# Performance work log

Hardware: AMD Instinct MI355X
Metric: run time of the kernel (lower is better)

Reference implementation:

```python
import jax, jax.numpy as jnp
import numpy as np

jax.config.update("jax_enable_x64", True)  # original torch code runs in float64; minors underflow fp32

D = 96   # Nsites
N = 48   # Nparticles


def setup_inputs() -> dict:
    key = jax.random.key(0)
    # Orthonormal single-particle orbitals (columns), as the module assumes (P^T P = I)
    A = jax.random.normal(key, (D, D), dtype=jnp.float64)
    Q, _ = jnp.linalg.qr(A)
    P = Q[:, :N]  # [D, N]
    # A valid ordered particle configuration: strictly increasing, occ_positions[k] <= D-N+k
    occ_positions = jnp.arange(N, dtype=jnp.int32) * (D // N)  # stride-2 filling
    return {"P": P, "occ_positions": occ_positions}


def _cond_probs(P, occ_positions):
    """Conditional probabilities probs[k, x] of placing the k-th (ordered) particle at
    site x given particles 0..k-1 at occ_positions[0..k-1].

    Math identical to SlaterDetSampler_ordered.get_cond_prob (naive_update=True):
      G = I - P P^T
      probs[k,x] = -det(M_x[0:x+1,0:x+1]) / det(M[0:xmin,0:xmin])
    where M = G - diag(occupancy of particles < k) and M_x additionally sets n_x = 1.
    Since Ksites is always the contiguous range 0..x, all determinants are LEADING
    principal minors; and because only the (x,x) diagonal entry changes by -1 (last index
    of the block), det(M_x block) = d_{x+1} - d_x with d_j the leading j-minor of M.
    """
    Dd, Nn = P.shape
    dt = P.dtype
    eye = jnp.eye(Dd, dtype=dt)
    G = eye - P @ P.T                                             # [D, D]

    onehots = jax.nn.one_hot(occ_positions, Dd, dtype=dt)         # [N, D]
    n_before = jnp.cumsum(onehots, axis=0) - onehots              # occupancy of particles < k
    A = G[None] - n_before[:, :, None] * eye                      # [N, D, D]: G - diag(n_<k)

    # All leading principal minors via batched det of masked matrices:
    # M_j = A on the [0:j,0:j] block, identity elsewhere  =>  det(M_j) = leading j-minor
    ii = jnp.arange(Dd)
    jj = jnp.arange(1, Dd + 1)
    blk = (ii[None, :, None] < jj[:, None, None]) & (ii[None, None, :] < jj[:, None, None])  # [D,D,D]
    Ms = jnp.where(blk[None], A[:, None], eye)                    # [N, D, D, D]
    d = jnp.linalg.det(Ms.reshape(Nn * Dd, Dd, Dd)).reshape(Nn, Dd)
    d_full = jnp.concatenate([jnp.ones((Nn, 1), dt), d], axis=1)  # d_full[k, j] = j-th leading minor

    k = jnp.arange(Nn)
    xmin = jnp.where(k == 0, 0, occ_positions[jnp.maximum(k - 1, 0)] + 1)  # [N]
    xmax = Dd - Nn + k + 1                                                  # [N]
    denom = jnp.take_along_axis(d_full, xmin[:, None], axis=1)              # [N, 1]
    num = d_full[:, 1:] - d_full[:, :-1]                                    # det(GG_num) per candidate x

    x = jnp.arange(Dd)
    support = (x[None, :] >= xmin[:, None]) & (x[None, :] < xmax[:, None])
    probs = jnp.where(support, -num / denom, jnp.zeros((), dt))
    # torch.where(abs(probs) > 1e-15, probs, 0.)
    probs = jnp.where(jnp.abs(probs) > 1e-15, probs, jnp.zeros((), dt))
    return probs


def reference(P, occ_positions):
    probs = _cond_probs(P, occ_positions)                          # [N, D]
    # prob of the full ordered sample = prod_k probs[k, occ_positions[k]]  (as in sample())
    p_k = jnp.take_along_axis(probs, occ_positions[:, None], axis=1)[:, 0]
    prob_sample = jnp.prod(p_k)
    return probs, prob_sample
```

## Files before the change

kernel.cpp:

```cpp
#include <hip/hip_runtime.h>
#include <math.h>

#define Dd 96
#define Nn 48
#define LD 97
#define PTS 98
#define WS_G_BYTES (Dd * Dd * 8)

__device__ __forceinline__ double frcp(double x) {
    double r = __builtin_amdgcn_rcp(x);
    r = fma(fma(-x, r, 1.0), r, r);
    r = fma(fma(-x, r, 1.0), r, r);
    return r;
}

__device__ __forceinline__ double rdlane(double v, int srcLane) {
    union { double d; int i[2]; } u; u.d = v;
    int lo = __builtin_amdgcn_readlane(u.i[0], srcLane);
    int hi = __builtin_amdgcn_readlane(u.i[1], srcLane);
    union { int i[2]; double d; } w; w.i[0] = lo; w.i[1] = hi;
    return w.d;
}

__global__ __launch_bounds__(256) void build_g(const float* __restrict__ P,
                                               double* __restrict__ Mg) {
    __shared__ float Ps[Dd * 48];
    const int t0 = threadIdx.x;
    for (int e = t0; e < Dd * 48; e += 256) Ps[e] = P[e];
    __syncthreads();
    const int e = blockIdx.x * 256 + t0;
    const int r = e / Dd, c = e - Dd * (e / Dd);
    const float* pr = Ps + r * 48;
    const float* pc = Ps + c * 48;
    double acc = 0.0;
#pragma unroll
    for (int t = 0; t < 48; ++t)
        acc -= (double)pr[t] * (double)pc[t];
    Mg[e] = acc;
}

__global__ __launch_bounds__(1024, 1) void slater_elim(const double* __restrict__ Mg,
                                                       const int* __restrict__ occ,
                                                       float* __restrict__ out,
                                                       unsigned* __restrict__ cnt) {
    __shared__ double Sbuf[4][6][Dd];
    __shared__ double ev16[16][6];
    __shared__ int    evmask16[16], sdead16[16];
    __shared__ double evm[6];
    __shared__ int    evmmask;
    __shared__ double gs_runprod;
    __shared__ int    gs_dead;
    __shared__ int    step_pub;
    __shared__ int    done4[4];
    __shared__ unsigned char flag[Dd];

    const int tid  = threadIdx.x;
    const int k    = blockIdx.x;
    const int n    = Dd - Nn + k + 1;
    const int lane = tid & 63;
    const int wave = tid >> 6;
    const int xmin = (k == 0) ? 0 : occ[k - 1] + 1;
    const int s_end = (n - 1) / 6;
    const int jend  = 6 * s_end;

    if (tid == 0) { step_pub = -1; gs_runprod = 1.0; gs_dead = 0; evmmask = 0; }
    if (tid < 4)  done4[tid] = 0;
    if (tid < 16) { evmask16[tid] = 0; sdead16[tid] = 0; }
    if (tid < Dd) flag[tid] = 0;
    __syncthreads();
    if (tid < k) flag[occ[tid]] = 1;
    __syncthreads();

    double myprob = 0.0;
    double rr[6][2];

#pragma unroll
    for (int u = 0; u < 6; ++u) {
        if (lane < 48) {
            const int row = 6 * wave + u;
            double2 g = *(const double2*)(Mg + row * Dd + 2 * lane);
            double d0 = (row == 2 * lane     && !flag[row]) ? 1.0 : 0.0;
            double d1 = (row == 2 * lane + 1 && !flag[row]) ? 1.0 : 0.0;
            rr[u][0] = g.x + d0;
            rr[u][1] = g.y + d1;
        } else { rr[u][0] = 0.0; rr[u][1] = 0.0; }
    }

    auto prefactor = [&](int p, int slot) {
        const int jb = 6 * p, jbH = 3 * p;
        double grun = gs_runprod; int gdead = gs_dead;
        int msk = 0;
#pragma unroll
        for (int cc = 0; cc < 6; ++cc) {
            const int src = jbH + (cc >> 1);
            double piv = rdlane(rr[cc][cc & 1], src);
            if (!gdead) {
                double ap = fabs(piv);
                int jj = jb + cc;
                if (jj >= xmin) {
                    if (lane == 0) ev16[p][cc] = grun * (1.0 - piv);
                    msk |= (1 << cc);
                    double nr = grun * piv;
                    if (!(ap > 1e-7) || !(ap < 8.0) || !(fabs(nr) > 1e-8)) gdead = 1;
                    else grun = nr;
                } else {
                    if (!(ap > 1e-12) || !(ap < 8.0)) gdead = 1;
                }
            }
            double rp = frcp(piv);
            rr[cc][0] *= rp; rr[cc][1] *= rp;
            if (cc < 5) {
                double f = rdlane(rr[cc + 1][cc & 1], src);
                rr[cc + 1][0] -= f * rr[cc][0];
                rr[cc + 1][1] -= f * rr[cc][1];
            }
#pragma unroll
            for (int i = 0; i < 6; ++i) {
                if (i == cc || i == cc + 1) continue;
                double f = rdlane(rr[i][cc & 1], src);
                rr[i][0] -= f * rr[cc][0];
                rr[i][1] -= f * rr[cc][1];
            }
        }
        if (lane == 0) {
            evmask16[p] = msk; sdead16[p] = gdead;
            gs_runprod = grun; gs_dead = gdead;
        }
        if (lane < 48) {
            const bool live = (2 * lane >= jb + 6);
#pragma unroll
            for (int r = 0; r < 6; ++r) {
                double2 sv;
                sv.x = live ? rr[r][0] : 0.0;
                sv.y = live ? rr[r][1] : 0.0;
                *(double2*)&Sbuf[slot][r][2 * lane] = sv;
            }
        }
        __threadfence_block();
        if (lane == 0)
            __hip_atomic_store(&step_pub, p, __ATOMIC_RELEASE, __HIP_MEMORY_SCOPE_WORKGROUP);
    };

    if (wave == 0) prefactor(0, 0);

    bool broke = false;
    const int smax = (wave < s_end) ? wave : s_end;
    for (int s = 0; s < smax; ++s) {
        while (__hip_atomic_load(&step_pub, __ATOMIC_ACQUIRE,
                                 __HIP_MEMORY_SCOPE_WORKGROUP) < s)
            __builtin_amdgcn_s_sleep(1);
        if (sdead16[s]) { broke = true; break; }
        const int slot = s & 3;
        double S0[6], S1[6];
        if (lane < 48) {
#pragma unroll
            for (int r = 0; r < 6; ++r) {
                double2 sv = *(const double2*)&Sbuf[slot][r][2 * lane];
                S0[r] = sv.x; S1[r] = sv.y;
            }
            const int al = 3 * s;
#pragma unroll
            for (int u = 0; u < 6; ++u) {
#pragma unroll
                for (int r = 0; r < 6; ++r) {
                    double a = rdlane(rr[u][r & 1], al + (r >> 1));
                    rr[u][0] -= a * S0[r];
                    rr[u][1] -= a * S1[r];
                }
            }
        }
        if (lane == 0)
            __hip_atomic_fetch_add(&done4[slot], 1, __ATOMIC_RELEASE,
                                   __HIP_MEMORY_SCOPE_WORKGROUP);
        if (wave == s + 1 && s + 1 < s_end) {
            const int p = s + 1;
            if (p >= 4) {
                const int q = p & 3, m = p >> 2;
                const int T = m * (15 - q) - 2 * m * (m - 1);
                while (__hip_atomic_load(&done4[q], __ATOMIC_ACQUIRE,
                                         __HIP_MEMORY_SCOPE_WORKGROUP) < T)
                    __builtin_amdgcn_s_sleep(1);
            }
            prefactor(p, p & 3);
        }
    }

    if (!broke && wave == s_end) {
        const int rsz = n - jend;
        double grun = gs_runprod; int gdead = gs_dead;
        int msk = 0;
#pragma unroll
        for (int cc = 0; cc < 6; ++cc) {
            const int src = 3 * s_end + (cc >> 1);
            double piv = rdlane(rr[cc][cc & 1], src);
            double evv = 0.0;
            if (cc < rsz - 1) {
                if (!gdead) {
                    double ap = fabs(piv);
                    int jj = jend + cc;
                    if (jj >= xmin) {
                        evv = grun * (1.0 - piv); msk |= (1 << cc);
                        double nr = grun * piv;
                        if (!(ap > 1e-7) || !(ap < 8.0) || !(fabs(nr) > 1e-8)) gdead = 1;
                        else grun = nr;
                    } else {
                        if (!(ap > 1e-12) || !(ap < 8.0)) gdead = 1;
                    }
                }
            } else if (cc == rsz - 1) {
                if (!gdead) { evv = grun * (1.0 - piv); msk |= (1 << cc); }
            }
            if (lane == 0) evm[cc] = evv;
            double rp = frcp(piv);
            rr[cc][0] *= rp; rr[cc][1] *= rp;
            if (cc < 5) {
                double f = rdlane(rr[cc + 1][cc & 1], src);
                rr[cc + 1][0] -= f * rr[cc][0];
                rr[cc + 1][1] -= f * rr[cc][1];
            }
#pragma unroll
            for (int i = 0; i < 6; ++i) {
                if (i == cc || i == cc + 1) continue;
                double f = rdlane(rr[i][cc & 1], src);
                rr[i][0] -= f * rr[cc][0];
                rr[i][1] -= f * rr[cc][1];
            }
        }
        if (lane == 0) evmmask = msk;
    }
    __syncthreads();

    if (tid < jend) {
        int sp = tid / 6, q = tid - 6 * sp;
        if ((evmask16[sp] >> q) & 1) myprob = ev16[sp][q];
    } else if (tid < n) {
        int q = tid - jend;
        if ((evmmask >> q) & 1) myprob = evm[q];
    }

    if (tid < Dd) {
        double p = myprob;
        if (!isfinite(p)) p = 0.0;
        if (!(fabs(p) > 1e-15)) p = 0.0;
        p = fmin(fmax(p, 0.0), 1.0);
        out[k * Dd + tid] = (float)p;
    }

    __threadfence();
    __syncthreads();
    if (wave == 0) {
        int old = 0;
        if (lane == 0)
            old = (int)__hip_atomic_fetch_add(cnt, 1u, __ATOMIC_ACQ_REL,
                                              __HIP_MEMORY_SCOPE_AGENT);
        old = __shfl(old, 0, 64);
        if (((unsigned)old + 1u) % (unsigned)Nn == 0u) {
            __threadfence();
            double v = 1.0;
            if (lane < Nn) {
                float f = __hip_atomic_load(out + lane * Dd + occ[lane],
                                            __ATOMIC_RELAXED, __HIP_MEMORY_SCOPE_AGENT);
                v = (double)f;
            }
#pragma unroll
            for (int off = 32; off >= 1; off >>= 1)
                v *= __shfl_down(v, off, 64);
            if (lane == 0) {
                if (!isfinite(v)) v = 0.0;
                out[Nn * Dd] = (float)v;
            }
        }
    }
}

__global__ __launch_bounds__(1024, 1) void slater_mono(const float* __restrict__ P,
                                                       const int* __restrict__ occ,
                                                       float* __restrict__ out,
                                                       unsigned* __restrict__ cnt) {
    __shared__ double As[Dd * LD];
    __shared__ double Sbuf[4][6][Dd];
    __shared__ double ev16[16][6];
    __shared__ int    evmask16[16], sdead16[16];
    __shared__ double evm[6];
    __shared__ int    evmmask;
    __shared__ double gs_runprod;
    __shared__ int    gs_dead;
    __shared__ int    step_pub;
    __shared__ int    done4[4];
    __shared__ unsigned char flag[Dd];
    float* PT = (float*)As;

    const int tid  = threadIdx.x;
    const int k    = blockIdx.x;
    const int n    = Dd - Nn + k + 1;
    const int lane = tid & 63;
    const int wave = tid >> 6;
    const int xmin = (k == 0) ? 0 : occ[k - 1] + 1;
    const int s_end = (n - 1) / 6;
    const int jend  = 6 * s_end;

    if (tid == 0) { step_pub = -1; gs_runprod = 1.0; gs_dead = 0; evmmask = 0; }
    if (tid < 4)  done4[tid] = 0;
    if (tid < 16) { evmask16[tid] = 0; sdead16[tid] = 0; }
    if (tid < Dd) flag[tid] = 0;
    __syncthreads();
    if (tid < k) flag[occ[tid]] = 1;
    for (int e = tid; e < Dd * Nn; e += 1024) {
        int c = e / Nn, t = e - (e / Nn) * Nn;
        PT[t * PTS + c] = P[e];
    }
    __syncthreads();

    double Areg[8]; int trs[2], tcs[2];
#pragma unroll
    for (int it = 0; it < 2; ++it) {
        int tau = tid + 1024 * it;
        double s00 = 0.0, s01 = 0.0, s10 = 0.0, s11 = 0.0;
        int tr = 0, tc = 0;
        if (tau < 1176) {
            tr = (int)((97.0 - sqrt(9409.0 - 8.0 * (double)tau)) * 0.5);
            while ((tr * (97 - tr)) / 2 > tau) --tr;
            while (((tr + 1) * (96 - tr)) / 2 <= tau) ++tr;
            tc = tr + (tau - (tr * (97 - tr)) / 2);
            int r0 = 2 * tr, c0 = 2 * tc;
            if (r0 < n && c0 < n) {
                for (int t = 0; t < Nn; ++t) {
                    const float* row = PT + t * PTS;
                    float2 pr = *(const float2*)(row + r0);
                    float2 pc = *(const float2*)(row + c0);
                    s00 -= (double)pr.x * (double)pc.x; s01 -= (double)pr.x * (double)pc.y;
                    s10 -= (double)pr.y * (double)pc.x; s11 -= (double)pr.y * (double)pc.y;
                }
            }
        }
        trs[it] = tr; tcs[it] = tc;
        Areg[it * 4 + 0] = s00; Areg[it * 4 + 1] = s01;
        Areg[it * 4 + 2] = s10; Areg[it * 4 + 3] = s11;
    }
    __syncthreads();
#pragma unroll
    for (int it = 0; it < 2; ++it) {
        int tau = tid + 1024 * it;
        if (tau < 1176) {
            int tr = trs[it], tc = tcs[it];
            int r0 = 2 * tr, c0 = 2 * tc;
            if (r0 < n && c0 < n) {
                bool r1 = (r0 + 1 < n), c1 = (c0 + 1 < n);
                double d0 = flag[r0] ? 0.0 : 1.0;
                double d1 = flag[r0 + 1] ? 0.0 : 1.0;
                As[r0 * LD + c0] = Areg[it * 4 + 0] + ((r0 == c0) ? d0 : 0.0);
                if (c1)       As[r0 * LD + c0 + 1]       = Areg[it * 4 + 1];
                if (r1)       As[(r0 + 1) * LD + c0]     = Areg[it * 4 + 2];
                if (r1 && c1) As[(r0 + 1) * LD + c0 + 1] = Areg[it * 4 + 3] + ((r0 == c0) ? d1 : 0.0);
                if (tr != tc) {
                    As[c0 * LD + r0] = Areg[it * 4 + 0];
                    if (c1)       As[(c0 + 1) * LD + r0]     = Areg[it * 4 + 1];
                    if (r1)       As[c0 * LD + r0 + 1]       = Areg[it * 4 + 2];
                    if (r1 && c1) As[(c0 + 1) * LD + r0 + 1] = Areg[it * 4 + 3];
                }
            }
        }
    }
    __syncthreads();

    double myprob = 0.0;
    double rr[6][2];
#pragma unroll
    for (int u = 0; u < 6; ++u) {
        if (lane < 48) {
            rr[u][0] = As[(6 * wave + u) * LD + 2 * lane];
            rr[u][1] = As[(6 * wave + u) * LD + 2 * lane + 1];
        } else { rr[u][0] = 0.0; rr[u][1] = 0.0; }
    }

    auto prefactor = [&](int p, int slot) {
        const int jb = 6 * p, jbH = 3 * p;
        double grun = gs_runprod; int gdead = gs_dead;
        int msk = 0;
#pragma unroll
        for (int cc = 0; cc < 6; ++cc) {
            const int src = jbH + (cc >> 1);
            double piv = rdlane(rr[cc][cc & 1], src);
            if (!gdead) {
                double ap = fabs(piv);
                int jj = jb + cc;
                if (jj >= xmin) {
                    if (lane == 0) ev16[p][cc] = grun * (1.0 - piv);
                    msk |= (1 << cc);
                    double nr = grun * piv;
                    if (!(ap > 1e-7) || !(ap < 8.0) || !(fabs(nr) > 1e-8)) gdead = 1;
                    else grun = nr;
                } else {
                    if (!(ap > 1e-12) || !(ap < 8.0)) gdead = 1;
                }
            }
            double rp = frcp(piv);
            rr[cc][0] *= rp; rr[cc][1] *= rp;
#pragma unroll
            for (int i = 0; i < 6; ++i) {
                if (i == cc) continue;
                double f = rdlane(rr[i][cc & 1], src);
                rr[i][0] -= f * rr[cc][0];
                rr[i][1] -= f * rr[cc][1];
            }
        }
        if (lane == 0) {
            evmask16[p] = msk; sdead16[p] = gdead;
            gs_runprod = grun; gs_dead = gdead;
        }
        if (lane < 48) {
            const bool live = (2 * lane >= jb + 6);
#pragma unroll
            for (int r = 0; r < 6; ++r) {
                double2 sv;
                sv.x = live ? rr[r][0] : 0.0;
                sv.y = live ? rr[r][1] : 0.0;
                *(double2*)&Sbuf[slot][r][2 * lane] = sv;
            }
        }
        __threadfence_block();
        if (lane == 0)
            __hip_atomic_store(&step_pub, p, __ATOMIC_RELEASE, __HIP_MEMORY_SCOPE_WORKGROUP);
    };

    if (wave == 0) prefactor(0, 0);

    bool broke = false;
    const int smax = (wave < s_end) ? wave : s_end;
    for (int s = 0; s < smax; ++s) {
        while (__hip_atomic_load(&step_pub, __ATOMIC_ACQUIRE,
                                 __HIP_MEMORY_SCOPE_WORKGROUP) < s)
            __builtin_amdgcn_s_sleep(1);
        if (sdead16[s]) { broke = true; break; }
        const int slot = s & 3;
        double S0[6], S1[6];
        if (lane < 48) {
#pragma unroll
            for (int r = 0; r < 6; ++r) {
                double2 sv = *(const double2*)&Sbuf[slot][r][2 * lane];
                S0[r] = sv.x; S1[r] = sv.y;
            }
        }
        asm volatile("s_waitcnt lgkmcnt(0)" ::: "memory");
        if (lane == 0)
            __hip_atomic_fetch_add(&done4[slot], 1, __ATOMIC_RELAXED,
                                   __HIP_MEMORY_SCOPE_WORKGROUP);
        if (lane < 48) {
            const int al = 3 * s;
#pragma unroll
            for (int u = 0; u < 6; ++u) {
#pragma unroll
                for (int r = 0; r < 6; ++r) {
                    double a = rdlane(rr[u][r & 1], al + (r >> 1));
                    rr[u][0] -= a * S0[r];
                    rr[u][1] -= a * S1[r];
                }
            }
        }
        if (wave == s + 1 && s + 1 < s_end) {
            const int p = s + 1;
            if (p >= 4) {
                const int q = p & 3, m = p >> 2;
                const int T = m * (15 - q) - 2 * m * (m - 1);
                while (__hip_atomic_load(&done4[q], __ATOMIC_ACQUIRE,
                                         __HIP_MEMORY_SCOPE_WORKGROUP) < T)
                    __builtin_amdgcn_s_sleep(1);
            }
            prefactor(p, p & 3);
        }
    }

    if (!broke && wave == s_end) {
        const int rsz = n - jend;
        double grun = gs_runprod; int gdead = gs_dead;
        int msk = 0;
#pragma unroll
        for (int cc = 0; cc < 6; ++cc) {
            const int src = 3 * s_end + (cc >> 1);
            double piv = rdlane(rr[cc][cc & 1], src);
            double evv = 0.0;
            if (cc < rsz - 1) {
                if (!gdead) {
                    double ap = fabs(piv);
                    int jj = jend + cc;
                    if (jj >= xmin) {
                        evv = grun * (1.0 - piv); msk |= (1 << cc);
                        double nr = grun * piv;
                        if (!(ap > 1e-7) || !(ap < 8.0) || !(fabs(nr) > 1e-8)) gdead = 1;
                        else grun = nr;
                    } else {
                        if (!(ap > 1e-12) || !(ap < 8.0)) gdead = 1;
                    }
                }
            } else if (cc == rsz - 1) {
                if (!gdead) { evv = grun * (1.0 - piv); msk |= (1 << cc); }
            }
            if (lane == 0) evm[cc] = evv;
            double rp = frcp(piv);
            rr[cc][0] *= rp; rr[cc][1] *= rp;
#pragma unroll
            for (int i = 0; i < 6; ++i) {
                if (i == cc) continue;
                double f = rdlane(rr[i][cc & 1], src);
                rr[i][0] -= f * rr[cc][0];
                rr[i][1] -= f * rr[cc][1];
            }
        }
        if (lane == 0) evmmask = msk;
    }
    __syncthreads();

    if (tid < jend) {
        int sp = tid / 6, q = tid - 6 * sp;
        if ((evmask16[sp] >> q) & 1) myprob = ev16[sp][q];
    } else if (tid < n) {
        int q = tid - jend;
        if ((evmmask >> q) & 1) myprob = evm[q];
    }

    if (tid < Dd) {
        double p = myprob;
        if (!isfinite(p)) p = 0.0;
        if (!(fabs(p) > 1e-15)) p = 0.0;
        p = fmin(fmax(p, 0.0), 1.0);
        out[k * Dd + tid] = (float)p;
    }

    __threadfence();
    __syncthreads();
    if (wave == 0) {
        int old = 0;
        if (lane == 0)
            old = (int)__hip_atomic_fetch_add(cnt, 1u, __ATOMIC_ACQ_REL,
                                              __HIP_MEMORY_SCOPE_AGENT);
        old = __shfl(old, 0, 64);
        if (((unsigned)old + 1u) % (unsigned)Nn == 0u) {
            __threadfence();
            double v = 1.0;
            if (lane < Nn) {
                float f = __hip_atomic_load(out + lane * Dd + occ[lane],
                                            __ATOMIC_RELAXED, __HIP_MEMORY_SCOPE_AGENT);
                v = (double)f;
            }
#pragma unroll
            for (int off = 32; off >= 1; off >>= 1)
                v *= __shfl_down(v, off, 64);
            if (lane == 0) {
                if (!isfinite(v)) v = 0.0;
                out[Nn * Dd] = (float)v;
            }
        }
    }
}

extern "C" void kernel_launch(void* const* d_in, const int* in_sizes, int n_in,
                              void* d_out, int out_size, void* d_ws, size_t ws_size,
                              hipStream_t stream) {
    const float* P = (const float*)d_in[0];
    const int* occ = (const int*)d_in[1];
    float* out = (float*)d_out;

    if (ws_size >= (size_t)(WS_G_BYTES + 16)) {
        double* Mg = (double*)d_ws;
        unsigned* cnt = (unsigned*)((char*)d_ws + WS_G_BYTES);
        build_g<<<36, 256, 0, stream>>>(P, Mg);
        slater_elim<<<Nn, 1024, 0, stream>>>(Mg, occ, out, cnt);
    } else {
        slater_mono<<<Nn, 1024, 0, stream>>>(P, occ, out, (unsigned*)d_ws);
    }
}
```

Before: 93.48 us.

## Use full 16-slot panel buffer, drop slot reuse counters, prioritize next pivot wave

The shared panel buffer grows from 4 ring slots to one slot per step, so the wave building the next panel no longer waits on per-slot completion counters before overwriting. The next-panel owner wave spin-waits without sleeping and raises its scheduling priority while it does its update and prefactor, which shortens the critical path of the wavefront pipeline. Other waves sleep longer while polling. The cost is more LDS use (about 74 KB for the buffer) and tighter spinning by one wave.

```diff
diff --git a/kernel.cpp b/kernel.cpp
--- a/kernel.cpp
+++ b/kernel.cpp
@@ -43,7 +43,7 @@
                                                        const int* __restrict__ occ,
                                                        float* __restrict__ out,
                                                        unsigned* __restrict__ cnt) {
-    __shared__ double Sbuf[4][6][Dd];
+    __shared__ double Sbuf[16][6][Dd];
     __shared__ double ev16[16][6];
     __shared__ int    evmask16[16], sdead16[16];
     __shared__ double evm[6];
@@ -51,7 +51,6 @@
     __shared__ double gs_runprod;
     __shared__ int    gs_dead;
     __shared__ int    step_pub;
-    __shared__ int    done4[4];
     __shared__ unsigned char flag[Dd];
 
     const int tid  = threadIdx.x;
@@ -64,7 +63,6 @@
     const int jend  = 6 * s_end;
 
     if (tid == 0) { step_pub = -1; gs_runprod = 1.0; gs_dead = 0; evmmask = 0; }
-    if (tid < 4)  done4[tid] = 0;
     if (tid < 16) { evmask16[tid] = 0; sdead16[tid] = 0; }
     if (tid < Dd) flag[tid] = 0;
     __syncthreads();
@@ -86,7 +84,7 @@
         } else { rr[u][0] = 0.0; rr[u][1] = 0.0; }
     }
 
-    auto prefactor = [&](int p, int slot) {
+    auto prefactor = [&](int p) {
         const int jb = 6 * p, jbH = 3 * p;
         double grun = gs_runprod; int gdead = gs_dead;
         int msk = 0;
@@ -133,7 +131,7 @@
                 double2 sv;
                 sv.x = live ? rr[r][0] : 0.0;
                 sv.y = live ? rr[r][1] : 0.0;
-                *(double2*)&Sbuf[slot][r][2 * lane] = sv;
+                *(double2*)&Sbuf[p][r][2 * lane] = sv;
             }
         }
         __threadfence_block();
@@ -141,21 +139,27 @@
             __hip_atomic_store(&step_pub, p, __ATOMIC_RELEASE, __HIP_MEMORY_SCOPE_WORKGROUP);
     };
 
-    if (wave == 0) prefactor(0, 0);
+    if (wave == 0) prefactor(0);
 
     bool broke = false;
     const int smax = (wave < s_end) ? wave : s_end;
     for (int s = 0; s < smax; ++s) {
-        while (__hip_atomic_load(&step_pub, __ATOMIC_ACQUIRE,
-                                 __HIP_MEMORY_SCOPE_WORKGROUP) < s)
-            __builtin_amdgcn_s_sleep(1);
+        const bool nextOwner = (wave == s + 1);
+        if (nextOwner) {
+            while (__hip_atomic_load(&step_pub, __ATOMIC_ACQUIRE,
+                                     __HIP_MEMORY_SCOPE_WORKGROUP) < s) {}
+        } else {
+            while (__hip_atomic_load(&step_pub, __ATOMIC_ACQUIRE,
+                                     __HIP_MEMORY_SCOPE_WORKGROUP) < s)
+                __builtin_amdgcn_s_sleep(2);
+        }
         if (sdead16[s]) { broke = true; break; }
-        const int slot = s & 3;
+        if (nextOwner) __builtin_amdgcn_s_setprio(1);
         double S0[6], S1[6];
         if (lane < 48) {
 #pragma unroll
             for (int r = 0; r < 6; ++r) {
-                double2 sv = *(const double2*)&Sbuf[slot][r][2 * lane];
+                double2 sv = *(const double2*)&Sbuf[s][r][2 * lane];
                 S0[r] = sv.x; S1[r] = sv.y;
             }
             const int al = 3 * s;
@@ -169,20 +173,9 @@
                 }
             }
         }
-        if (lane == 0)
-            __hip_atomic_fetch_add(&done4[slot], 1, __ATOMIC_RELEASE,
-                                   __HIP_MEMORY_SCOPE_WORKGROUP);
-        if (wave == s + 1 && s + 1 < s_end) {
-            const int p = s + 1;
-            if (p >= 4) {
-                const int q = p & 3, m = p >> 2;
-                const int T = m * (15 - q) - 2 * m * (m - 1);
-                while (__hip_atomic_load(&done4[q], __ATOMIC_ACQUIRE,
-                                         __HIP_MEMORY_SCOPE_WORKGROUP) < T)
-                    __builtin_amdgcn_s_sleep(1);
-            }
-            prefactor(p, p & 3);
-        }
+        if (nextOwner && s + 1 < s_end)
+            prefactor(s + 1);
+        if (nextOwner) __builtin_amdgcn_s_setprio(0);
     }
 
     if (!broke && wave == s_end) {
```

Result: faster. 90.90 us (median of 2 runs) (-2.8%).
